# Optimization experiments

Hardware: AMD Instinct MI355X
Metric: run time of the kernel (lower is better)

## Reference

```python
import jax, jax.numpy as jnp
import numpy as np

B, T, C = 4, 2048, 1024
H = 16
HD = C // H  # 64


def setup_inputs() -> dict:
    key = jax.random.key(0)
    ks = jax.random.split(key, 4)
    x = jax.random.normal(ks[0], (B, T, C), dtype=jnp.float32)
    # c_attn: Linear(C, 3C, bias=False)  (qkv_bias=False)
    w_attn = jax.random.normal(ks[1], (C, 3 * C), dtype=jnp.float32) / np.sqrt(C)
    # c_proj: Linear(C, C) with bias (nn.Linear default)
    w_proj = jax.random.normal(ks[2], (C, C), dtype=jnp.float32) / np.sqrt(C)
    b_proj = jax.random.normal(ks[3], (C,), dtype=jnp.float32) * 0.01
    return {"x": x, "w_attn": w_attn, "w_proj": w_proj, "b_proj": b_proj}


def reference(x, w_attn, w_proj, b_proj):
    b, t, c = x.shape
    qkv = x @ w_attn  # [B,T,3C]
    q, k, v = jnp.split(qkv, 3, axis=-1)
    # [B,H,T,HD]
    q = q.reshape(b, t, H, HD).transpose(0, 2, 1, 3)
    k = k.reshape(b, t, H, HD).transpose(0, 2, 1, 3)
    v = v.reshape(b, t, H, HD).transpose(0, 2, 1, 3)
    scale = 1.0 / np.sqrt(HD)
    attn = jnp.einsum('bhqd,bhkd->bhqk', q, k) * scale  # [B,H,T,T]
    causal = jnp.tril(jnp.ones((t, t), dtype=bool))
    attn = jnp.where(causal, attn, -jnp.inf)
    attn = jax.nn.softmax(attn, axis=-1)
    out = jnp.einsum('bhqk,bhkd->bhqd', attn, v)  # [B,H,T,HD]
    out = out.transpose(0, 2, 1, 3).reshape(b, t, c)
    return out @ w_proj + b_proj
```

## Files before the change

### kernel.cpp

```cpp
#include <hip/hip_runtime.h>

#define BB 4
#define TT 2048
#define CC 1024
#define C3 3072
#define HH 16
#define HD 64
#define BT 8192

#define TS 32
#define TSZ (64 * TS)

typedef __bf16 bf16x8 __attribute__((ext_vector_type(8)));
typedef float floatx4 __attribute__((ext_vector_type(4)));
typedef unsigned uintx2 __attribute__((ext_vector_type(2)));
typedef unsigned short u16;

__device__ __forceinline__ u16 f2bf(float f) {
  union { float f; unsigned u; } a; a.f = f;
  return (u16)((a.u + 0x7fffu + ((a.u >> 16) & 1u)) >> 16);
}
__device__ __forceinline__ bf16x8 ld8(const u16* p) { return *(const bf16x8*)p; }
__device__ __forceinline__ floatx4 mfma16(bf16x8 a, bf16x8 b, floatx4 c) {
  return __builtin_amdgcn_mfma_f32_16x16x32_bf16(a, b, c, 0, 0, 0);
}

__device__ __forceinline__ void gload16(const u16* g, u16* l) {
  __builtin_amdgcn_global_load_lds(
      (const __attribute__((address_space(1))) void*)g,
      (__attribute__((address_space(3))) void*)l, 16, 0, 0);
}

__device__ __forceinline__ void qd_xchg(unsigned a, unsigned b,
                                        unsigned& r0, unsigned& r1) {
  uintx2 t = __builtin_amdgcn_permlane32_swap(a, b, false, false);
  uintx2 r = __builtin_amdgcn_permlane16_swap(t[0], t[1], false, false);
  r0 = r[0]; r1 = r[1];
}

__global__ __launch_bounds__(256) void tobf16_kernel(const float4* __restrict__ src,
                                                     ushort4* __restrict__ dst, int n4) {
  int i = blockIdx.x * 256 + threadIdx.x;
  if (i >= n4) return;
  float4 v = src[i];
  ushort4 o; o.x = f2bf(v.x); o.y = f2bf(v.y); o.z = f2bf(v.z); o.w = f2bf(v.w);
  dst[i] = o;
}

__global__ __launch_bounds__(256) void transpose_bf16_kernel(const float* __restrict__ src,
                                                             u16* __restrict__ dst,
                                                             int K, int N) {
  __shared__ float s[64][65];
  const int t = threadIdx.x;
  const int r = t >> 4;
  const int c = (t & 15) * 4;
  const int k0 = blockIdx.y * 64, n0 = blockIdx.x * 64;
#pragma unroll
  for (int i = 0; i < 4; ++i) {
    float4 v = *(const float4*)&src[(size_t)(k0 + r + i * 16) * N + n0 + c];
    s[r + i * 16][c + 0] = v.x; s[r + i * 16][c + 1] = v.y;
    s[r + i * 16][c + 2] = v.z; s[r + i * 16][c + 3] = v.w;
  }
  __syncthreads();
#pragma unroll
  for (int i = 0; i < 4; ++i) {
    const int nn = r + i * 16;
    ushort4 o;
    o.x = f2bf(s[c + 0][nn]); o.y = f2bf(s[c + 1][nn]);
    o.z = f2bf(s[c + 2][nn]); o.w = f2bf(s[c + 3][nn]);
    *(ushort4*)&dst[(size_t)(n0 + nn) * K + k0 + c] = o;
  }
}

template<int MODE>
__global__ __launch_bounds__(256) void gemm_kernel(
    const u16* __restrict__ A, const u16* __restrict__ B,
    const float* __restrict__ bias, float* __restrict__ outf,
    u16* __restrict__ qk, u16* __restrict__ vT,
    int M, int N, int K) {
  __shared__ u16 smem[2][2][2 * TSZ];

  const int t = threadIdx.x;
  const int w = t >> 6, lane = t & 63, lr = lane & 15, qd = lane >> 4;
  const int wm = w >> 1, wn = w & 1;
  const int m0 = blockIdx.y * 128, n0 = blockIdx.x * 128;

  const int sr = t >> 2;
  const int sc = (t & 3) * 8;
  const int wb = (t & ~63) * 8;
  const u16* Ag = A + (size_t)(m0 + sr) * K + sc;
  const u16* Bg = B + (size_t)(n0 + sr) * K + sc;

  floatx4 acc[4][4] = {};

  {
    u16* sA = &smem[0][0][0];
    u16* sB = &smem[0][1][0];
    gload16(Ag,                  &sA[wb]);
    gload16(Ag + (size_t)64 * K, &sA[TSZ + wb]);
    gload16(Bg,                  &sB[wb]);
    gload16(Bg + (size_t)64 * K, &sB[TSZ + wb]);
  }
  __syncthreads();

  for (int k0 = 0; k0 < K; k0 += 32) {
    const int p = (k0 >> 5) & 1;
    if (k0 + 32 < K) {
      u16* sA = &smem[p ^ 1][0][0];
      u16* sB = &smem[p ^ 1][1][0];
      gload16(Ag + k0 + 32,                  &sA[wb]);
      gload16(Ag + (size_t)64 * K + k0 + 32, &sA[TSZ + wb]);
      gload16(Bg + k0 + 32,                  &sB[wb]);
      gload16(Bg + (size_t)64 * K + k0 + 32, &sB[TSZ + wb]);
    }
    const u16* sA = &smem[p][0][0];
    const u16* sB = &smem[p][1][0];

    bf16x8 af[4], bf[4];
#pragma unroll
    for (int mj = 0; mj < 4; ++mj) af[mj] = ld8(&sA[(wm * 64 + mj * 16 + lr) * TS + qd * 8]);
#pragma unroll
    for (int nj = 0; nj < 4; ++nj) bf[nj] = ld8(&sB[(wn * 64 + nj * 16 + lr) * TS + qd * 8]);
#pragma unroll
    for (int mj = 0; mj < 4; ++mj)
#pragma unroll
      for (int nj = 0; nj < 4; ++nj)
        acc[mj][nj] = mfma16(af[mj], bf[nj], acc[mj][nj]);
    __syncthreads();
  }

  const int rowg0 = m0 + wm * 64;
  const int colg0 = n0 + wn * 64;
  if constexpr (MODE == 2) {
#pragma unroll
    for (int nj = 0; nj < 4; ++nj) {
      const int col = colg0 + nj * 16 + lr;
      const float bv = bias[col];
#pragma unroll
      for (int mj = 0; mj < 4; ++mj)
#pragma unroll
        for (int i = 0; i < 4; ++i)
          outf[(size_t)(rowg0 + mj * 16 + qd * 4 + i) * N + col] = acc[mj][nj][i] + bv;
    }
  } else {
    u16* Tw = &smem[0][0][0] + w * (32 * 72);
    const bool isV = (n0 >= 2 * CC);
    if (!isV) {
      const float qs = (n0 < CC) ? 0.18033688011f : 1.0f;
#pragma unroll
      for (int half = 0; half < 2; ++half) {
#pragma unroll
        for (int m2 = 0; m2 < 2; ++m2)
#pragma unroll
          for (int nj = 0; nj < 4; ++nj)
#pragma unroll
            for (int i = 0; i < 4; ++i)
              Tw[(m2 * 16 + qd * 4 + i) * 72 + nj * 16 + lr] =
                  f2bf(acc[half * 2 + m2][nj][i] * qs);
#pragma unroll
        for (int s = 0; s < 4; ++s) {
          const int rl = s * 8 + (lane >> 3);
          const int c0 = (lane & 7) * 8;
          *(bf16x8*)&qk[(size_t)(rowg0 + half * 32 + rl) * (2 * CC) + colg0 + c0] =
              ld8(&Tw[rl * 72 + c0]);
        }
      }
    } else {
      const int bI = m0 >> 11;
      const int tbase = (m0 & (TT - 1)) + wm * 64;
      const int dim0 = colg0 - 2 * CC;
#pragma unroll
      for (int half = 0; half < 2; ++half) {
#pragma unroll
        for (int n2 = 0; n2 < 2; ++n2)
#pragma unroll
          for (int mj = 0; mj < 4; ++mj)
#pragma unroll
            for (int i = 0; i < 4; ++i)
              Tw[(n2 * 16 + lr) * 72 + mj * 16 + qd * 4 + i] =
                  f2bf(acc[mj][half * 2 + n2][i]);
#pragma unroll
        for (int s = 0; s < 4; ++s) {
          const int dl = s * 8 + (lane >> 3);
          const int t0 = (lane & 7) * 8;
          *(bf16x8*)&vT[((size_t)(bI << 10) + dim0 + half * 32 + dl) * TT + tbase + t0] =
              ld8(&Tw[dl * 72 + t0]);
        }
      }
    }
  }
}

__global__ __launch_bounds__(256, 5) void attn_kernel(const u16* __restrict__ qk,
                                                      const u16* __restrict__ vT,
                                                      u16* __restrict__ att) {
  __shared__ u16 sKV[2][4][TSZ];

  const int t = threadIdx.x;
  const int w = t >> 6, lane = t & 63, lr = lane & 15, qd = lane >> 4;
  const int qtile = 31 - blockIdx.y;
  const int bh = blockIdx.x;
  const int b = bh >> 4, h = bh & 15;
  const int q0 = qtile * 64;
  const u16* qbase = qk + (size_t)b * TT * (2 * CC);

  const u16* qp = qbase + (size_t)(q0 + w * 16 + lr) * (2 * CC) + h * HD;
  const bf16x8 qf0 = ld8(qp + qd * 8);
  const bf16x8 qf1 = ld8(qp + 32 + qd * 8);

  const int sr = t >> 2, sc = (t & 3) * 8;
  const int wb = (t & ~63) * 8;
  const u16* Kg = qbase + (size_t)sr * (2 * CC) + CC + h * HD + sc;
  const u16* Vg = vT + ((size_t)bh * HD + sr) * TT + sc;

  float lsum = 0.f;
  floatx4 o[4] = {};
  const int myq = q0 + w * 16 + lr;

  {
    u16* b0 = &sKV[0][0][0];
    gload16(Kg,      &b0[wb]);
    gload16(Kg + 32, &b0[TSZ + wb]);
    gload16(Vg,      &b0[2 * TSZ + wb]);
    gload16(Vg + 32, &b0[3 * TSZ + wb]);
  }
  __syncthreads();

  for (int kt = 0; kt <= qtile; ++kt) {
    if (kt < qtile) {
      const int kn = (kt + 1) * 64;
      u16* bn = &sKV[(kt + 1) & 1][0][0];
      gload16(Kg + (size_t)kn * (2 * CC),      &bn[wb]);
      gload16(Kg + (size_t)kn * (2 * CC) + 32, &bn[TSZ + wb]);
      gload16(Vg + kn,                         &bn[2 * TSZ + wb]);
      gload16(Vg + kn + 32,                    &bn[3 * TSZ + wb]);
    }

    const u16* sK0 = &sKV[kt & 1][0][0];
    const u16* sK1 = &sKV[kt & 1][1][0];
    const u16* sV0 = &sKV[kt & 1][2][0];
    const u16* sV1 = &sKV[kt & 1][3][0];

    floatx4 s[4] = {};
#pragma unroll
    for (int j = 0; j < 4; ++j) {
      bf16x8 kf0 = ld8(&sK0[(j * 16 + lr) * TS + qd * 8]);
      bf16x8 kf1 = ld8(&sK1[(j * 16 + lr) * TS + qd * 8]);
      s[j] = mfma16(kf0, qf0, s[j]);
      s[j] = mfma16(kf1, qf1, s[j]);
    }

    const bool diag = (kt == qtile);
    unsigned W[4][2];
#pragma unroll
    for (int j = 0; j < 4; ++j) {
      float p[4];
#pragma unroll
      for (int i = 0; i < 4; ++i) {
        p[i] = __builtin_amdgcn_exp2f(s[j][i]);
        if (diag) {
          const int key = kt * 64 + j * 16 + qd * 4 + i;
          p[i] = (key <= myq) ? p[i] : 0.f;
        }
        lsum += p[i];
      }
      W[j][0] = __builtin_amdgcn_perm(__float_as_uint(p[1]), __float_as_uint(p[0]), 0x07060302);
      W[j][1] = __builtin_amdgcn_perm(__float_as_uint(p[3]), __float_as_uint(p[2]), 0x07060302);
    }

    uint4 F0, F1;
    qd_xchg(W[0][0], W[1][0], F0.x, F0.z);
    qd_xchg(W[0][1], W[1][1], F0.y, F0.w);
    qd_xchg(W[2][0], W[3][0], F1.x, F1.z);
    qd_xchg(W[2][1], W[3][1], F1.y, F1.w);
    const bf16x8 pf0 = __builtin_bit_cast(bf16x8, F0);
    const bf16x8 pf1 = __builtin_bit_cast(bf16x8, F1);

#pragma unroll
    for (int j = 0; j < 4; ++j) {
      bf16x8 vf0 = ld8(&sV0[(j * 16 + lr) * TS + qd * 8]);
      bf16x8 vf1 = ld8(&sV1[(j * 16 + lr) * TS + qd * 8]);
      o[j] = mfma16(pf0, vf0, o[j]);
      o[j] = mfma16(pf1, vf1, o[j]);
    }
    __syncthreads();
  }

  lsum += __shfl_xor(lsum, 16);
  lsum += __shfl_xor(lsum, 32);
  float linv[4];
#pragma unroll
  for (int i = 0; i < 4; ++i) linv[i] = 1.0f / __shfl(lsum, qd * 4 + i);

#pragma unroll
  for (int j = 0; j < 4; ++j)
#pragma unroll
    for (int i = 0; i < 4; ++i) {
      const size_t row = (size_t)b * TT + q0 + w * 16 + qd * 4 + i;
      att[row * CC + h * HD + j * 16 + lr] = f2bf(o[j][i] * linv[i]);
    }
}

extern "C" void kernel_launch(void* const* d_in, const int* in_sizes, int n_in,
                              void* d_out, int out_size, void* d_ws, size_t ws_size,
                              hipStream_t stream) {
  const float* x      = (const float*)d_in[0];
  const float* w_attn = (const float*)d_in[1];
  const float* w_proj = (const float*)d_in[2];
  const float* b_proj = (const float*)d_in[3];
  float* out = (float*)d_out;

  char* ws = (char*)d_ws;
  u16* xb  = (u16*)(ws + 0);
  u16* waT = (u16*)(ws + 16777216);
  u16* wpT = (u16*)(ws + 23068672);
  u16* qk  = (u16*)(ws + 25165824);
  u16* vT  = (u16*)(ws + 58720256);
  u16* att = (u16*)(ws + 75497472);

  tobf16_kernel<<<8192, 256, 0, stream>>>((const float4*)x, (ushort4*)xb, 2097152);
  transpose_bf16_kernel<<<dim3(48, 16), 256, 0, stream>>>(w_attn, waT, CC, C3);
  transpose_bf16_kernel<<<dim3(16, 16), 256, 0, stream>>>(w_proj, wpT, CC, CC);

  gemm_kernel<1><<<dim3(24, 64), 256, 0, stream>>>(xb, waT, nullptr, nullptr, qk, vT,
                                                   BT, C3, CC);
  attn_kernel<<<dim3(64, 32), 256, 0, stream>>>(qk, vT, att);

  gemm_kernel<2><<<dim3(8, 64), 256, 0, stream>>>(att, wpT, b_proj, out, nullptr, nullptr,
                                                  BT, CC, CC);
}
```

Measured before the change: 236.2 us.

## Fuse prep kernels, retile QKV GEMM with swizzle, pair causal q-tiles

Merges the x conversion and both weight transposes into a single prep launch. Replaces the QKV GEMM with a 512-thread 256x128-tile kernel using an XOR-swizzled shared-memory layout to reduce bank conflicts. Each attention block now processes a short and a long q-tile in sequence to balance causal work, halving the grid. This trades fewer blocks and larger tiles for possible occupancy loss.

```diff
diff --git a/kernel.cpp b/kernel.cpp
--- a/kernel.cpp
+++ b/kernel.cpp
@@ -38,23 +38,31 @@
   r0 = r[0]; r1 = r[1];
 }
 
-__global__ __launch_bounds__(256) void tobf16_kernel(const float4* __restrict__ src,
-                                                     ushort4* __restrict__ dst, int n4) {
-  int i = blockIdx.x * 256 + threadIdx.x;
-  if (i >= n4) return;
-  float4 v = src[i];
-  ushort4 o; o.x = f2bf(v.x); o.y = f2bf(v.y); o.z = f2bf(v.z); o.w = f2bf(v.w);
-  dst[i] = o;
-}
-
-__global__ __launch_bounds__(256) void transpose_bf16_kernel(const float* __restrict__ src,
-                                                             u16* __restrict__ dst,
-                                                             int K, int N) {
+__global__ __launch_bounds__(256) void prep_kernel(
+    const float4* __restrict__ x4, ushort4* __restrict__ xb4,
+    const float* __restrict__ w_attn, u16* __restrict__ waT,
+    const float* __restrict__ w_proj, u16* __restrict__ wpT) {
   __shared__ float s[64][65];
   const int t = threadIdx.x;
+  const int bid = blockIdx.x;
+
+  if (bid < 8192) {
+    const int i = bid * 256 + t;
+    float4 v = x4[i];
+    ushort4 o; o.x = f2bf(v.x); o.y = f2bf(v.y); o.z = f2bf(v.z); o.w = f2bf(v.w);
+    xb4[i] = o;
+    return;
+  }
+
+  const float* src; u16* dst; int N, bx, by;
+  if (bid < 8960) { const int b2 = bid - 8192; src = w_attn; dst = waT; N = C3;
+                    bx = b2 % 48; by = b2 / 48; }
+  else            { const int b2 = bid - 8960; src = w_proj; dst = wpT; N = CC;
+                    bx = b2 % 16; by = b2 / 16; }
+  const int K = CC;
   const int r = t >> 4;
   const int c = (t & 15) * 4;
-  const int k0 = blockIdx.y * 64, n0 = blockIdx.x * 64;
+  const int k0 = by * 64, n0 = bx * 64;
 #pragma unroll
   for (int i = 0; i < 4; ++i) {
     float4 v = *(const float4*)&src[(size_t)(k0 + r + i * 16) * N + n0 + c];
@@ -72,11 +80,116 @@
   }
 }
 
-template<int MODE>
+__global__ __launch_bounds__(512, 4) void qkv_kernel(
+    const u16* __restrict__ A, const u16* __restrict__ B,
+    u16* __restrict__ qk, u16* __restrict__ vT, int K) {
+  __shared__ u16 smem[2][12288];
+
+  const int t = threadIdx.x;
+  const int lane = t & 63, lr = lane & 15, qd = lane >> 4;
+  const int w = t >> 6, wm = w >> 1, wn = w & 1;
+  const int m0 = blockIdx.y * 256, n0 = blockIdx.x * 128;
+
+  const int sr = t >> 2;
+  const int scol = ((t & 3) ^ (sr & 3)) * 8;
+  const int wb = (t & ~63) * 8;
+  const u16* Ag = A + (size_t)(m0 + sr) * K + scol;
+  const u16* Bg = B + (size_t)(n0 + sr) * K + scol;
+
+  floatx4 acc[4][4] = {};
+
+  {
+    u16* sA = &smem[0][0];
+    u16* sB = &smem[0][8192];
+    gload16(Ag,                    &sA[wb]);
+    gload16(Ag + (size_t)128 * K,  &sA[4096 + wb]);
+    gload16(Bg,                    &sB[wb]);
+  }
+  __syncthreads();
+
+  const int csw = ((qd ^ (lr & 3))) * 8;
+
+  for (int k0 = 0; k0 < K; k0 += 32) {
+    const int p = (k0 >> 5) & 1;
+    if (k0 + 32 < K) {
+      u16* sA = &smem[p ^ 1][0];
+      u16* sB = &smem[p ^ 1][8192];
+      gload16(Ag + k0 + 32,                   &sA[wb]);
+      gload16(Ag + (size_t)128 * K + k0 + 32, &sA[4096 + wb]);
+      gload16(Bg + k0 + 32,                   &sB[wb]);
+    }
+    const u16* sA = &smem[p][0];
+    const u16* sB = &smem[p][8192];
+
+    bf16x8 af[4], bf[4];
+#pragma unroll
+    for (int mi = 0; mi < 4; ++mi)
+      af[mi] = ld8(&sA[(wm * 64 + mi * 16 + lr) * 32 + csw]);
+#pragma unroll
+    for (int nj = 0; nj < 4; ++nj)
+      bf[nj] = ld8(&sB[(wn * 64 + nj * 16 + lr) * 32 + csw]);
+#pragma unroll
+    for (int mi = 0; mi < 4; ++mi)
+#pragma unroll
+      for (int nj = 0; nj < 4; ++nj)
+        acc[mi][nj] = mfma16(af[mi], bf[nj], acc[mi][nj]);
+    __syncthreads();
+  }
+
+  u16* flat = &smem[0][0];
+  const int rowg0 = m0 + wm * 64;
+  const int colg0 = n0 + wn * 64;
+  const bool isV = (n0 >= 2 * CC);
+  if (!isV) {
+    const float qs = (n0 < CC) ? 0.18033688011f : 1.0f;
+    u16* Tw = flat + w * (32 * 72);
+#pragma unroll
+    for (int half = 0; half < 2; ++half) {
+#pragma unroll
+      for (int m2 = 0; m2 < 2; ++m2)
+#pragma unroll
+        for (int nj = 0; nj < 4; ++nj)
+#pragma unroll
+          for (int i = 0; i < 4; ++i)
+            Tw[(m2 * 16 + qd * 4 + i) * 72 + nj * 16 + lr] =
+                f2bf(acc[half * 2 + m2][nj][i] * qs);
+#pragma unroll
+      for (int s = 0; s < 4; ++s) {
+        const int rl = s * 8 + (lane >> 3);
+        const int c0 = (lane & 7) * 8;
+        *(bf16x8*)&qk[(size_t)(rowg0 + half * 32 + rl) * (2 * CC) + colg0 + c0] =
+            ld8(&Tw[rl * 72 + c0]);
+      }
+    }
+  } else {
+    u16* Tw = flat + w * (32 * 72);
+    const int bI = m0 >> 11;
+    const int tbase = (m0 & (TT - 1)) + wm * 64;
+    const int dim0 = colg0 - 2 * CC;
+#pragma unroll
+    for (int half = 0; half < 2; ++half) {
+#pragma unroll
+      for (int n2 = 0; n2 < 2; ++n2)
+#pragma unroll
+        for (int mj = 0; mj < 4; ++mj)
+#pragma unroll
+          for (int i = 0; i < 4; ++i)
+            Tw[(n2 * 16 + lr) * 72 + mj * 16 + qd * 4 + i] =
+                f2bf(acc[mj][half * 2 + n2][i]);
+#pragma unroll
+      for (int s = 0; s < 4; ++s) {
+        const int dl = s * 8 + (lane >> 3);
+        const int t0 = (lane & 7) * 8;
+        *(bf16x8*)&vT[((size_t)(bI << 10) + dim0 + half * 32 + dl) * TT + tbase + t0] =
+            ld8(&Tw[dl * 72 + t0]);
+      }
+    }
+  }
+}
+
 __global__ __launch_bounds__(256) void gemm_kernel(
     const u16* __restrict__ A, const u16* __restrict__ B,
     const float* __restrict__ bias, float* __restrict__ outf,
-    u16* __restrict__ qk, u16* __restrict__ vT,
     int M, int N, int K) {
   __shared__ u16 smem[2][2][2 * TSZ];
 
@@ -131,63 +244,15 @@
 
   const int rowg0 = m0 + wm * 64;
   const int colg0 = n0 + wn * 64;
-  if constexpr (MODE == 2) {
-#pragma unroll
-    for (int nj = 0; nj < 4; ++nj) {
-      const int col = colg0 + nj * 16 + lr;
-      const float bv = bias[col];
-#pragma unroll
-      for (int mj = 0; mj < 4; ++mj)
-#pragma unroll
-        for (int i = 0; i < 4; ++i)
-          outf[(size_t)(rowg0 + mj * 16 + qd * 4 + i) * N + col] = acc[mj][nj][i] + bv;
-    }
-  } else {
-    u16* Tw = &smem[0][0][0] + w * (32 * 72);
-    const bool isV = (n0 >= 2 * CC);
-    if (!isV) {
-      const float qs = (n0 < CC) ? 0.18033688011f : 1.0f;
-#pragma unroll
-      for (int half = 0; half < 2; ++half) {
-#pragma unroll
-        for (int m2 = 0; m2 < 2; ++m2)
-#pragma unroll
-          for (int nj = 0; nj < 4; ++nj)
-#pragma unroll
-            for (int i = 0; i < 4; ++i)
-              Tw[(m2 * 16 + qd * 4 + i) * 72 + nj * 16 + lr] =
-                  f2bf(acc[half * 2 + m2][nj][i] * qs);
-#pragma unroll
-        for (int s = 0; s < 4; ++s) {
-          const int rl = s * 8 + (lane >> 3);
-          const int c0 = (lane & 7) * 8;
-          *(bf16x8*)&qk[(size_t)(rowg0 + half * 32 + rl) * (2 * CC) + colg0 + c0] =
-              ld8(&Tw[rl * 72 + c0]);
-        }
-      }
-    } else {
-      const int bI = m0 >> 11;
-      const int tbase = (m0 & (TT - 1)) + wm * 64;
-      const int dim0 = colg0 - 2 * CC;
-#pragma unroll
-      for (int half = 0; half < 2; ++half) {
-#pragma unroll
-        for (int n2 = 0; n2 < 2; ++n2)
-#pragma unroll
-          for (int mj = 0; mj < 4; ++mj)
-#pragma unroll
-            for (int i = 0; i < 4; ++i)
-              Tw[(n2 * 16 + lr) * 72 + mj * 16 + qd * 4 + i] =
-                  f2bf(acc[mj][half * 2 + n2][i]);
-#pragma unroll
-        for (int s = 0; s < 4; ++s) {
-          const int dl = s * 8 + (lane >> 3);
-          const int t0 = (lane & 7) * 8;
-          *(bf16x8*)&vT[((size_t)(bI << 10) + dim0 + half * 32 + dl) * TT + tbase + t0] =
-              ld8(&Tw[dl * 72 + t0]);
-        }
-      }
-    }
+#pragma unroll
+  for (int nj = 0; nj < 4; ++nj) {
+    const int col = colg0 + nj * 16 + lr;
+    const float bv = bias[col];
+#pragma unroll
+    for (int mj = 0; mj < 4; ++mj)
+#pragma unroll
+      for (int i = 0; i < 4; ++i)
+        outf[(size_t)(rowg0 + mj * 16 + qd * 4 + i) * N + col] = acc[mj][nj][i] + bv;
   }
 }
 
@@ -198,107 +263,111 @@
 
   const int t = threadIdx.x;
   const int w = t >> 6, lane = t & 63, lr = lane & 15, qd = lane >> 4;
-  const int qtile = 31 - blockIdx.y;
   const int bh = blockIdx.x;
   const int b = bh >> 4, h = bh & 15;
-  const int q0 = qtile * 64;
   const u16* qbase = qk + (size_t)b * TT * (2 * CC);
-
-  const u16* qp = qbase + (size_t)(q0 + w * 16 + lr) * (2 * CC) + h * HD;
-  const bf16x8 qf0 = ld8(qp + qd * 8);
-  const bf16x8 qf1 = ld8(qp + 32 + qd * 8);
 
   const int sr = t >> 2, sc = (t & 3) * 8;
   const int wb = (t & ~63) * 8;
   const u16* Kg = qbase + (size_t)sr * (2 * CC) + CC + h * HD + sc;
   const u16* Vg = vT + ((size_t)bh * HD + sr) * TT + sc;
 
-  float lsum = 0.f;
-  floatx4 o[4] = {};
-  const int myq = q0 + w * 16 + lr;
-
-  {
-    u16* b0 = &sKV[0][0][0];
-    gload16(Kg,      &b0[wb]);
-    gload16(Kg + 32, &b0[TSZ + wb]);
-    gload16(Vg,      &b0[2 * TSZ + wb]);
-    gload16(Vg + 32, &b0[3 * TSZ + wb]);
-  }
-  __syncthreads();
-
-  for (int kt = 0; kt <= qtile; ++kt) {
-    if (kt < qtile) {
-      const int kn = (kt + 1) * 64;
-      u16* bn = &sKV[(kt + 1) & 1][0][0];
-      gload16(Kg + (size_t)kn * (2 * CC),      &bn[wb]);
-      gload16(Kg + (size_t)kn * (2 * CC) + 32, &bn[TSZ + wb]);
-      gload16(Vg + kn,                         &bn[2 * TSZ + wb]);
-      gload16(Vg + kn + 32,                    &bn[3 * TSZ + wb]);
-    }
-
-    const u16* sK0 = &sKV[kt & 1][0][0];
-    const u16* sK1 = &sKV[kt & 1][1][0];
-    const u16* sV0 = &sKV[kt & 1][2][0];
-    const u16* sV1 = &sKV[kt & 1][3][0];
-
-    floatx4 s[4] = {};
-#pragma unroll
-    for (int j = 0; j < 4; ++j) {
-      bf16x8 kf0 = ld8(&sK0[(j * 16 + lr) * TS + qd * 8]);
-      bf16x8 kf1 = ld8(&sK1[(j * 16 + lr) * TS + qd * 8]);
-      s[j] = mfma16(kf0, qf0, s[j]);
-      s[j] = mfma16(kf1, qf1, s[j]);
-    }
-
-    const bool diag = (kt == qtile);
-    unsigned W[4][2];
-#pragma unroll
-    for (int j = 0; j < 4; ++j) {
-      float p[4];
+#pragma unroll 1
+  for (int pass = 0; pass < 2; ++pass) {
+    const int qtile = pass ? (31 - blockIdx.y) : blockIdx.y;
+    const int q0 = qtile * 64;
+
+    const u16* qp = qbase + (size_t)(q0 + w * 16 + lr) * (2 * CC) + h * HD;
+    const bf16x8 qf0 = ld8(qp + qd * 8);
+    const bf16x8 qf1 = ld8(qp + 32 + qd * 8);
+
+    float lsum = 0.f;
+    floatx4 o[4] = {};
+    const int myq = q0 + w * 16 + lr;
+
+    {
+      u16* b0 = &sKV[0][0][0];
+      gload16(Kg,      &b0[wb]);
+      gload16(Kg + 32, &b0[TSZ + wb]);
+      gload16(Vg,      &b0[2 * TSZ + wb]);
+      gload16(Vg + 32, &b0[3 * TSZ + wb]);
+    }
+    __syncthreads();
+
+    for (int kt = 0; kt <= qtile; ++kt) {
+      if (kt < qtile) {
+        const int kn = (kt + 1) * 64;
+        u16* bn = &sKV[(kt + 1) & 1][0][0];
+        gload16(Kg + (size_t)kn * (2 * CC),      &bn[wb]);
+        gload16(Kg + (size_t)kn * (2 * CC) + 32, &bn[TSZ + wb]);
+        gload16(Vg + kn,                         &bn[2 * TSZ + wb]);
+        gload16(Vg + kn + 32,                    &bn[3 * TSZ + wb]);
+      }
+
+      const u16* sK0 = &sKV[kt & 1][0][0];
+      const u16* sK1 = &sKV[kt & 1][1][0];
+      const u16* sV0 = &sKV[kt & 1][2][0];
+      const u16* sV1 = &sKV[kt & 1][3][0];
+
+      floatx4 s[4] = {};
+#pragma unroll
+      for (int j = 0; j < 4; ++j) {
+        bf16x8 kf0 = ld8(&sK0[(j * 16 + lr) * TS + qd * 8]);
+        bf16x8 kf1 = ld8(&sK1[(j * 16 + lr) * TS + qd * 8]);
+        s[j] = mfma16(kf0, qf0, s[j]);
+        s[j] = mfma16(kf1, qf1, s[j]);
+      }
+
+      const bool diag = (kt == qtile);
+      unsigned W[4][2];
+#pragma unroll
+      for (int j = 0; j < 4; ++j) {
+        float p[4];
+#pragma unroll
+        for (int i = 0; i < 4; ++i) {
+          p[i] = __builtin_amdgcn_exp2f(s[j][i]);
+          if (diag) {
+            const int key = kt * 64 + j * 16 + qd * 4 + i;
+            p[i] = (key <= myq) ? p[i] : 0.f;
+          }
+          lsum += p[i];
+        }
+        W[j][0] = __builtin_amdgcn_perm(__float_as_uint(p[1]), __float_as_uint(p[0]), 0x07060302);
+        W[j][1] = __builtin_amdgcn_perm(__float_as_uint(p[3]), __float_as_uint(p[2]), 0x07060302);
+      }
+
+      uint4 F0, F1;
+      qd_xchg(W[0][0], W[1][0], F0.x, F0.z);
+      qd_xchg(W[0][1], W[1][1], F0.y, F0.w);
+      qd_xchg(W[2][0], W[3][0], F1.x, F1.z);
+      qd_xchg(W[2][1], W[3][1], F1.y, F1.w);
+      const bf16x8 pf0 = __builtin_bit_cast(bf16x8, F0);
+      const bf16x8 pf1 = __builtin_bit_cast(bf16x8, F1);
+
+#pragma unroll
+      for (int j = 0; j < 4; ++j) {
+        bf16x8 vf0 = ld8(&sV0[(j * 16 + lr) * TS + qd * 8]);
+        bf16x8 vf1 = ld8(&sV1[(j * 16 + lr) * TS + qd * 8]);
+        o[j] = mfma16(pf0, vf0, o[j]);
+        o[j] = mfma16(pf1, vf1, o[j]);
+      }
+      __syncthreads();
+    }
+
+    lsum += __shfl_xor(lsum, 16);
+    lsum += __shfl_xor(lsum, 32);
+    float linv[4];
+#pragma unroll
+    for (int i = 0; i < 4; ++i) linv[i] = 1.0f / __shfl(lsum, qd * 4 + i);
+
+#pragma unroll
+    for (int j = 0; j < 4; ++j)
 #pragma unroll
       for (int i = 0; i < 4; ++i) {
-        p[i] = __builtin_amdgcn_exp2f(s[j][i]);
-        if (diag) {
-          const int key = kt * 64 + j * 16 + qd * 4 + i;
-          p[i] = (key <= myq) ? p[i] : 0.f;
-        }
-        lsum += p[i];
-      }
-      W[j][0] = __builtin_amdgcn_perm(__float_as_uint(p[1]), __float_as_uint(p[0]), 0x07060302);
-      W[j][1] = __builtin_amdgcn_perm(__float_as_uint(p[3]), __float_as_uint(p[2]), 0x07060302);
-    }
-
-    uint4 F0, F1;
-    qd_xchg(W[0][0], W[1][0], F0.x, F0.z);
-    qd_xchg(W[0][1], W[1][1], F0.y, F0.w);
-    qd_xchg(W[2][0], W[3][0], F1.x, F1.z);
-    qd_xchg(W[2][1], W[3][1], F1.y, F1.w);
-    const bf16x8 pf0 = __builtin_bit_cast(bf16x8, F0);
-    const bf16x8 pf1 = __builtin_bit_cast(bf16x8, F1);
-
-#pragma unroll
-    for (int j = 0; j < 4; ++j) {
-      bf16x8 vf0 = ld8(&sV0[(j * 16 + lr) * TS + qd * 8]);
-      bf16x8 vf1 = ld8(&sV1[(j * 16 + lr) * TS + qd * 8]);
-      o[j] = mfma16(pf0, vf0, o[j]);
-      o[j] = mfma16(pf1, vf1, o[j]);
-    }
-    __syncthreads();
-  }
-
-  lsum += __shfl_xor(lsum, 16);
-  lsum += __shfl_xor(lsum, 32);
-  float linv[4];
-#pragma unroll
-  for (int i = 0; i < 4; ++i) linv[i] = 1.0f / __shfl(lsum, qd * 4 + i);
-
-#pragma unroll
-  for (int j = 0; j < 4; ++j)
-#pragma unroll
-    for (int i = 0; i < 4; ++i) {
-      const size_t row = (size_t)b * TT + q0 + w * 16 + qd * 4 + i;
-      att[row * CC + h * HD + j * 16 + lr] = f2bf(o[j][i] * linv[i]);
-    }
+        const size_t row = (size_t)b * TT + q0 + w * 16 + qd * 4 + i;
+        att[row * CC + h * HD + j * 16 + lr] = f2bf(o[j][i] * linv[i]);
+      }
+  }
 }
 
 extern "C" void kernel_launch(void* const* d_in, const int* in_sizes, int n_in,
@@ -318,14 +387,13 @@
   u16* vT  = (u16*)(ws + 58720256);
   u16* att = (u16*)(ws + 75497472);
 
-  tobf16_kernel<<<8192, 256, 0, stream>>>((const float4*)x, (ushort4*)xb, 2097152);
-  transpose_bf16_kernel<<<dim3(48, 16), 256, 0, stream>>>(w_attn, waT, CC, C3);
-  transpose_bf16_kernel<<<dim3(16, 16), 256, 0, stream>>>(w_proj, wpT, CC, CC);
-
-  gemm_kernel<1><<<dim3(24, 64), 256, 0, stream>>>(xb, waT, nullptr, nullptr, qk, vT,
-                                                   BT, C3, CC);
-  attn_kernel<<<dim3(64, 32), 256, 0, stream>>>(qk, vT, att);
-
-  gemm_kernel<2><<<dim3(8, 64), 256, 0, stream>>>(att, wpT, b_proj, out, nullptr, nullptr,
-                                                  BT, CC, CC);
-}
+  prep_kernel<<<9216, 256, 0, stream>>>((const float4*)x, (ushort4*)xb,
+                                        w_attn, waT, w_proj, wpT);
+
+  qkv_kernel<<<dim3(24, 32), 512, 0, stream>>>(xb, waT, qk, vT, CC);
+
+  attn_kernel<<<dim3(64, 16), 256, 0, stream>>>(qk, vT, att);
+
+  gemm_kernel<<<dim3(8, 64), 256, 0, stream>>>(att, wpT, b_proj, out,
+                                               BT, CC, CC);
+}
```

Result: faster. 229.3 us (-2.9%).
